# Optimization experiments

Hardware: AMD Instinct MI355X
Metric: run time of the kernel (lower is better)

## Reference

```python
import jax, jax.numpy as jnp
import numpy as np

FP8_MAX = 448.0


def _quantize_fp8(x):
    """Per-tensor symmetric quantization matching the Triton kernel's decode.

    Encode: u = round(clip(x*scale, -448, 448) / 448 * 127)  (stored as u+128 in uint8)
    Decode: x_hat = u / 127 * 448 / scale,  with scale = 448 / amax(|x|).
    We keep u as a float array of integers in [-127, 127] (the +128 uint8 bias
    cancels in the kernel's `u - 128`).
    """
    amax = jnp.max(jnp.abs(x))
    scale = FP8_MAX / jnp.maximum(amax, jnp.asarray(1e-12, x.dtype))
    q = jnp.clip(x * scale, -FP8_MAX, FP8_MAX)
    u = jnp.round(q / FP8_MAX * 127.0)
    return u, scale


def reference(x, weight):
    orig_shape = x.shape
    K = weight.shape[1]
    x2d = x.reshape(-1, K)                      # [M, K]

    ua, a_scale = _quantize_fp8(x2d)            # codes + per-tensor scale
    uw, w_scale = _quantize_fp8(weight)         # weight: [N, K]

    # Kernel dequant: val = u / 127 * FP8_MAX; acc in fp32; rescale by 1/(a_scale*b_scale)
    a_f = ua * (FP8_MAX / 127.0)
    b_f = (uw * (FP8_MAX / 127.0)).T            # [K, N] (weight_fp8.t())
    acc = a_f @ b_f                              # fp32 accumulate, [M, N]
    out = acc * (1.0 / (a_scale * w_scale))
    out = out.astype(x.dtype)
    return out.reshape(*orig_shape[:-1], weight.shape[0])


def setup_inputs() -> dict:
    key = jax.random.key(0)
    k1, k2 = jax.random.split(key)
    x = jax.random.normal(k1, (4, 2048, 4096), dtype=jnp.float32)
    weight = jax.random.normal(k2, (8192, 4096), dtype=jnp.float32) * 0.02
    return {"x": x, "weight": weight}
```

## Files before the change

### kernel.cpp

```cpp
#include <hip/hip_runtime.h>

#define FP8_MAX_F 448.0f

static constexpr int M = 8192;
static constexpr int N = 8192;
static constexpr int K = 4096;

typedef __attribute__((ext_vector_type(4))) int i32x4;

#define AS1 __attribute__((address_space(1)))
#define AS3 __attribute__((address_space(3)))
#define BARRIER() asm volatile("s_barrier" ::: "memory")
#define VMCNT(n)  asm volatile("s_waitcnt vmcnt(" #n ")" ::: "memory")

__global__ void amax_kernel(const float* __restrict__ x, const float* __restrict__ w,
                            unsigned* __restrict__ out) {
    const long n4x = (long)M * K / 4;
    const long n4t = n4x + (long)N * K / 4;
    unsigned lx = 0u, lw = 0u;
    const long stride = (long)gridDim.x * blockDim.x;
    for (long i = (long)blockIdx.x * blockDim.x + threadIdx.x; i < n4t; i += stride) {
        if (i < n4x) {
            float4 v = ((const float4*)x)[i];
            unsigned a0 = __float_as_uint(v.x) & 0x7fffffffu;
            unsigned a1 = __float_as_uint(v.y) & 0x7fffffffu;
            unsigned a2 = __float_as_uint(v.z) & 0x7fffffffu;
            unsigned a3 = __float_as_uint(v.w) & 0x7fffffffu;
            lx = max(lx, max(max(a0, a1), max(a2, a3)));
        } else {
            float4 v = ((const float4*)w)[i - n4x];
            unsigned a0 = __float_as_uint(v.x) & 0x7fffffffu;
            unsigned a1 = __float_as_uint(v.y) & 0x7fffffffu;
            unsigned a2 = __float_as_uint(v.z) & 0x7fffffffu;
            unsigned a3 = __float_as_uint(v.w) & 0x7fffffffu;
            lw = max(lw, max(max(a0, a1), max(a2, a3)));
        }
    }
    #pragma unroll
    for (int off = 32; off > 0; off >>= 1) {
        lx = max(lx, (unsigned)__shfl_down((int)lx, off, 64));
        lw = max(lw, (unsigned)__shfl_down((int)lw, off, 64));
    }
    __shared__ unsigned smx[4], smw[4];
    if ((threadIdx.x & 63) == 0) { smx[threadIdx.x >> 6] = lx; smw[threadIdx.x >> 6] = lw; }
    __syncthreads();
    if (threadIdx.x == 0) {
        atomicMax(&out[0], max(max(smx[0], smx[1]), max(smx[2], smx[3])));
        atomicMax(&out[1], max(max(smw[0], smw[1]), max(smw[2], smw[3])));
    }
}

__device__ __forceinline__ signed char quant1(float v, float s) {
    float f = fminf(fmaxf(v * s, -FP8_MAX_F), FP8_MAX_F);
    return (signed char)(int)rintf(f / FP8_MAX_F * 127.0f);
}

__global__ void quant_kernel(const float* __restrict__ x, const float* __restrict__ w,
                             signed char* __restrict__ qx, signed char* __restrict__ qw,
                             const unsigned* __restrict__ amax_bits) {
    const float ax = fmaxf(__uint_as_float(amax_bits[0]), 1e-12f);
    const float aw = fmaxf(__uint_as_float(amax_bits[1]), 1e-12f);
    const float sxv = FP8_MAX_F / ax;
    const float swv = FP8_MAX_F / aw;
    const long cx = (long)M * K / 16;
    const long ct = cx + (long)N * K / 16;
    const long stride = (long)gridDim.x * blockDim.x;
    for (long ci = (long)blockIdx.x * blockDim.x + threadIdx.x; ci < ct; ci += stride) {
        const float* src; signed char* dst; float s; long c;
        if (ci < cx) { src = x; dst = qx; s = sxv; c = ci; }
        else         { src = w; dst = qw; s = swv; c = ci - cx; }
        const long r = c >> 8;
        const int  cr = (int)(c & 255);
        const float4* in = (const float4*)(src + r * K + cr * 16);
        signed char ob[16];
        #pragma unroll
        for (int j = 0; j < 4; ++j) {
            float4 v = in[j];
            ob[j * 4 + 0] = quant1(v.x, s);
            ob[j * 4 + 1] = quant1(v.y, s);
            ob[j * 4 + 2] = quant1(v.z, s);
            ob[j * 4 + 3] = quant1(v.w, s);
        }
        const int osub = (cr & 3) ^ ((int)(r >> 1) & 3);
        *(int4*)(dst + r * K + ((long)((cr & ~3) + osub)) * 16) = *(const int4*)ob;
    }
}

__global__ __launch_bounds__(512, 2) void gemm_i8_kernel(
    const signed char* __restrict__ Aq, const signed char* __restrict__ Bq,
    float* __restrict__ C, const unsigned* __restrict__ amax_bits)
{
    __shared__ signed char lds[4][2][256 * 64];

    const int tid  = threadIdx.x;
    const int wid  = tid >> 6;
    const int lane = tid & 63;
    const int wm = wid >> 2;
    const int wn = wid & 3;
    const int fr = lane & 15;
    const int fq = lane >> 4;

    const long row0 = (long)blockIdx.x * 256;
    const long col0 = (long)blockIdx.y * 256;

    const signed char* Ablk = Aq + row0 * K;
    const signed char* Bblk = Bq + col0 * K;

    const long stag_off = (long)(tid >> 2) * K + (long)(tid & 3) * 16;

    const int arow = wm * 128 + fr;
    const int aoff = arow * 64 + ((fq ^ ((arow >> 1) & 3)) * 16);
    const int brow = wn * 64 + fr;
    const int boff = brow * 64 + ((fq ^ ((brow >> 1) & 3)) * 16);

    i32x4 acc[8][4] = {};
    i32x4 afR[2][8];
    i32x4 bR[2][4];

#define STAGE_AB(st) do { \
        const signed char* ga = Ablk + (long)(st) * 64 + stag_off; \
        const signed char* gb = Bblk + (long)(st) * 64 + stag_off; \
        signed char* lA = &lds[(st) & 3][0][0]; \
        signed char* lB = &lds[(st) & 3][1][0]; \
        __builtin_amdgcn_global_load_lds((const AS1 void*)ga, \
            (AS3 void*)(lA + wid * 1024), 16, 0, 0); \
        __builtin_amdgcn_global_load_lds((const AS1 void*)(ga + 128L * K), \
            (AS3 void*)(lA + 8192 + wid * 1024), 16, 0, 0); \
        __builtin_amdgcn_global_load_lds((const AS1 void*)gb, \
            (AS3 void*)(lB + wid * 1024), 16, 0, 0); \
        __builtin_amdgcn_global_load_lds((const AS1 void*)(gb + 128L * K), \
            (AS3 void*)(lB + 8192 + wid * 1024), 16, 0, 0); \
    } while (0)

#define READS(t1, NXT) do { \
        const signed char* la = &lds[(t1) & 3][0][0]; \
        const signed char* lb = &lds[(t1) & 3][1][0]; \
        _Pragma("unroll") \
        for (int mi = 0; mi < 8; ++mi) \
            afR[NXT][mi] = *(const i32x4*)(la + aoff + mi * 1024); \
        _Pragma("unroll") \
        for (int ni = 0; ni < 4; ++ni) \
            bR[NXT][ni] = *(const i32x4*)(lb + boff + ni * 1024); \
    } while (0)

#define MFMA32(CUR) do { \
        BARRIER(); \
        __builtin_amdgcn_s_setprio(1); \
        _Pragma("unroll") \
        for (int mi = 0; mi < 8; ++mi) { \
            _Pragma("unroll") \
            for (int ni = 0; ni < 4; ++ni) \
                acc[mi][ni] = __builtin_amdgcn_mfma_i32_16x16x64_i8( \
                    afR[CUR][mi], bR[CUR][ni], acc[mi][ni], 0, 0, 0); \
        } \
        __builtin_amdgcn_s_setprio(0); \
        BARRIER(); \
    } while (0)

    STAGE_AB(0); STAGE_AB(1); STAGE_AB(2);
    VMCNT(4);
    BARRIER();
    READS(0, 0);

    #pragma unroll 1
    for (int t = 0; t < 60; t += 2) {
        READS(t + 1, 1);
        STAGE_AB(t + 3);
        VMCNT(4);
        MFMA32(0);

        READS(t + 2, 0);
        STAGE_AB(t + 4);
        VMCNT(4);
        MFMA32(1);
    }
    READS(61, 1); STAGE_AB(63); VMCNT(4); MFMA32(0);
    READS(62, 0);               VMCNT(0); MFMA32(1);
    READS(63, 1);                         MFMA32(0);
    MFMA32(1);

#undef MFMA32
#undef READS
#undef STAGE_AB

    const float ax = fmaxf(__uint_as_float(amax_bits[0]), 1e-12f);
    const float aw = fmaxf(__uint_as_float(amax_bits[1]), 1e-12f);
    const float factor = ax * aw * (1.0f / (127.0f * 127.0f));

    #pragma unroll
    for (int mi = 0; mi < 8; ++mi) {
        #pragma unroll
        for (int ni = 0; ni < 4; ++ni) {
            const long col = col0 + wn * 64 + ni * 16 + fr;
            #pragma unroll
            for (int j = 0; j < 4; ++j) {
                const long row = row0 + wm * 128 + mi * 16 + fq * 4 + j;
                C[row * N + col] = (float)acc[mi][ni][j] * factor;
            }
        }
    }
}

extern "C" void kernel_launch(void* const* d_in, const int* in_sizes, int n_in,
                              void* d_out, int out_size, void* d_ws, size_t ws_size,
                              hipStream_t stream) {
    const float* x = (const float*)d_in[0];
    const float* w = (const float*)d_in[1];
    float* out = (float*)d_out;

    unsigned char* ws = (unsigned char*)d_ws;
    unsigned* amax = (unsigned*)ws;
    signed char* aq = (signed char*)(ws + 256);
    signed char* wq = aq + (long)M * K;

    hipMemsetAsync(amax, 0, 2 * sizeof(unsigned), stream);
    amax_kernel<<<2048, 256, 0, stream>>>(x, w, amax);
    quant_kernel<<<4096, 256, 0, stream>>>(x, w, aq, wq, amax);

    dim3 grid(M / 256, N / 256);
    gemm_i8_kernel<<<grid, 512, 0, stream>>>(aq, wq, out, amax);
}
```

Baseline: 442.5 us.

## Interleave LDS reads and global stages across four MFMA clusters per tile

Splits each 32-MFMA tile into four 8-MFMA clusters, each with its own barriers. The LDS fragment reads for the next tile and the A/B global-to-LDS stage issues are spread between these clusters instead of being issued in one burst before the MFMA block. Barriers are wrapped in sched_barrier so the compiler cannot move instructions across them. The aim is finer overlap of LDS and global traffic with MFMA work, at the cost of four times as many workgroup barriers per tile.

```diff
diff --git a/kernel.cpp b/kernel.cpp
--- a/kernel.cpp
+++ b/kernel.cpp
@@ -10,7 +10,11 @@
 
 #define AS1 __attribute__((address_space(1)))
 #define AS3 __attribute__((address_space(3)))
-#define BARRIER() asm volatile("s_barrier" ::: "memory")
+#define BARRIER() do { \
+        __builtin_amdgcn_sched_barrier(0); \
+        asm volatile("s_barrier" ::: "memory"); \
+        __builtin_amdgcn_sched_barrier(0); \
+    } while (0)
 #define VMCNT(n)  asm volatile("s_waitcnt vmcnt(" #n ")" ::: "memory")
 
 __global__ void amax_kernel(const float* __restrict__ x, const float* __restrict__ w,
@@ -117,71 +121,96 @@
     i32x4 afR[2][8];
     i32x4 bR[2][4];
 
-#define STAGE_AB(st) do { \
+#define STAGE_A(st) do { \
         const signed char* ga = Ablk + (long)(st) * 64 + stag_off; \
-        const signed char* gb = Bblk + (long)(st) * 64 + stag_off; \
         signed char* lA = &lds[(st) & 3][0][0]; \
-        signed char* lB = &lds[(st) & 3][1][0]; \
         __builtin_amdgcn_global_load_lds((const AS1 void*)ga, \
             (AS3 void*)(lA + wid * 1024), 16, 0, 0); \
         __builtin_amdgcn_global_load_lds((const AS1 void*)(ga + 128L * K), \
             (AS3 void*)(lA + 8192 + wid * 1024), 16, 0, 0); \
+    } while (0)
+
+#define STAGE_B(st) do { \
+        const signed char* gb = Bblk + (long)(st) * 64 + stag_off; \
+        signed char* lB = &lds[(st) & 3][1][0]; \
         __builtin_amdgcn_global_load_lds((const AS1 void*)gb, \
             (AS3 void*)(lB + wid * 1024), 16, 0, 0); \
         __builtin_amdgcn_global_load_lds((const AS1 void*)(gb + 128L * K), \
             (AS3 void*)(lB + 8192 + wid * 1024), 16, 0, 0); \
     } while (0)
 
-#define READS(t1, NXT) do { \
-        const signed char* la = &lds[(t1) & 3][0][0]; \
-        const signed char* lb = &lds[(t1) & 3][1][0]; \
-        _Pragma("unroll") \
-        for (int mi = 0; mi < 8; ++mi) \
-            afR[NXT][mi] = *(const i32x4*)(la + aoff + mi * 1024); \
-        _Pragma("unroll") \
-        for (int ni = 0; ni < 4; ++ni) \
-            bR[NXT][ni] = *(const i32x4*)(lb + boff + ni * 1024); \
-    } while (0)
-
-#define MFMA32(CUR) do { \
+#define CLUSTER(CUR, P) do { \
         BARRIER(); \
         __builtin_amdgcn_s_setprio(1); \
         _Pragma("unroll") \
-        for (int mi = 0; mi < 8; ++mi) { \
-            _Pragma("unroll") \
-            for (int ni = 0; ni < 4; ++ni) \
-                acc[mi][ni] = __builtin_amdgcn_mfma_i32_16x16x64_i8( \
-                    afR[CUR][mi], bR[CUR][ni], acc[mi][ni], 0, 0, 0); \
+        for (int ni = 0; ni < 4; ++ni) { \
+            acc[2*(P)][ni]   = __builtin_amdgcn_mfma_i32_16x16x64_i8( \
+                afR[CUR][2*(P)],   bR[CUR][ni], acc[2*(P)][ni],   0, 0, 0); \
+            acc[2*(P)+1][ni] = __builtin_amdgcn_mfma_i32_16x16x64_i8( \
+                afR[CUR][2*(P)+1], bR[CUR][ni], acc[2*(P)+1][ni], 0, 0, 0); \
         } \
         __builtin_amdgcn_s_setprio(0); \
         BARRIER(); \
     } while (0)
 
-    STAGE_AB(0); STAGE_AB(1); STAGE_AB(2);
+#define TILE_P(CUR, NXT, T1, S0_STMT, S1_STMT, VM_STMT, DO_RD) do { \
+        const signed char* la_ = &lds[(T1) & 3][0][0]; \
+        const signed char* lb_ = &lds[(T1) & 3][1][0]; \
+        if (DO_RD) { \
+            afR[NXT][0] = *(const i32x4*)(la_ + aoff + 0 * 1024); \
+            afR[NXT][1] = *(const i32x4*)(la_ + aoff + 1 * 1024); \
+        } \
+        S0_STMT; \
+        CLUSTER(CUR, 0); \
+        if (DO_RD) { \
+            afR[NXT][2] = *(const i32x4*)(la_ + aoff + 2 * 1024); \
+            afR[NXT][3] = *(const i32x4*)(la_ + aoff + 3 * 1024); \
+            bR[NXT][0]  = *(const i32x4*)(lb_ + boff + 0 * 1024); \
+        } \
+        S1_STMT; \
+        CLUSTER(CUR, 1); \
+        if (DO_RD) { \
+            afR[NXT][4] = *(const i32x4*)(la_ + aoff + 4 * 1024); \
+            afR[NXT][5] = *(const i32x4*)(la_ + aoff + 5 * 1024); \
+            bR[NXT][1]  = *(const i32x4*)(lb_ + boff + 1 * 1024); \
+        } \
+        CLUSTER(CUR, 2); \
+        if (DO_RD) { \
+            afR[NXT][6] = *(const i32x4*)(la_ + aoff + 6 * 1024); \
+            afR[NXT][7] = *(const i32x4*)(la_ + aoff + 7 * 1024); \
+            bR[NXT][2]  = *(const i32x4*)(lb_ + boff + 2 * 1024); \
+            bR[NXT][3]  = *(const i32x4*)(lb_ + boff + 3 * 1024); \
+        } \
+        VM_STMT; \
+        CLUSTER(CUR, 3); \
+    } while (0)
+
+    STAGE_A(0); STAGE_B(0);
+    STAGE_A(1); STAGE_B(1);
+    STAGE_A(2); STAGE_B(2);
     VMCNT(4);
     BARRIER();
-    READS(0, 0);
+    #pragma unroll
+    for (int mi = 0; mi < 8; ++mi)
+        afR[0][mi] = *(const i32x4*)(&lds[0][0][0] + aoff + mi * 1024);
+    #pragma unroll
+    for (int ni = 0; ni < 4; ++ni)
+        bR[0][ni] = *(const i32x4*)(&lds[0][1][0] + boff + ni * 1024);
 
     #pragma unroll 1
     for (int t = 0; t < 60; t += 2) {
-        READS(t + 1, 1);
-        STAGE_AB(t + 3);
-        VMCNT(4);
-        MFMA32(0);
-
-        READS(t + 2, 0);
-        STAGE_AB(t + 4);
-        VMCNT(4);
-        MFMA32(1);
-    }
-    READS(61, 1); STAGE_AB(63); VMCNT(4); MFMA32(0);
-    READS(62, 0);               VMCNT(0); MFMA32(1);
-    READS(63, 1);                         MFMA32(0);
-    MFMA32(1);
-
-#undef MFMA32
-#undef READS
-#undef STAGE_AB
+        TILE_P(0, 1, t + 1, STAGE_A(t + 3), STAGE_B(t + 3), VMCNT(4), 1);
+        TILE_P(1, 0, t + 2, STAGE_A(t + 4), STAGE_B(t + 4), VMCNT(4), 1);
+    }
+    TILE_P(0, 1, 61, STAGE_A(63), STAGE_B(63), VMCNT(4), 1);
+    TILE_P(1, 0, 62, (void)0,     (void)0,     VMCNT(0), 1);
+    TILE_P(0, 1, 63, (void)0,     (void)0,     (void)0,  1);
+    TILE_P(1, 0, 63, (void)0,     (void)0,     (void)0,  0);
+
+#undef TILE_P
+#undef CLUSTER
+#undef STAGE_B
+#undef STAGE_A
 
     const float ax = fmaxf(__uint_as_float(amax_bits[0]), 1e-12f);
     const float aw = fmaxf(__uint_as_float(amax_bits[1]), 1e-12f);
```

New measurement: 419.3 us. 1.06x faster.

## Shrink GEMM tile to 128x256 with double-buffered LDS for higher occupancy

Applied to the files above, without the earlier changes.

The int8 GEMM block tile goes from 256x256 to 128x256, and the 4-stage LDS ring becomes a 2-buffer ping-pong with a simpler stage/read/MFMA step per tile. Launch bounds target 4 blocks per CU, cutting per-wave accumulators from 32 to 16 MFMA tiles so more waves can hide latency. Each step now waits for all loads (vmcnt 0), so less prefetch depth and less data reuse per block. The amax reduction grid is also doubled.

```diff
diff --git a/kernel.cpp b/kernel.cpp
--- a/kernel.cpp
+++ b/kernel.cpp
@@ -86,11 +86,11 @@
     }
 }
 
-__global__ __launch_bounds__(512, 2) void gemm_i8_kernel(
+__global__ __launch_bounds__(512, 4) void gemm_i8_kernel(
     const signed char* __restrict__ Aq, const signed char* __restrict__ Bq,
     float* __restrict__ C, const unsigned* __restrict__ amax_bits)
 {
-    __shared__ signed char lds[4][2][256 * 64];
+    __shared__ signed char lds[2][24576];
 
     const int tid  = threadIdx.x;
     const int wid  = tid >> 6;
@@ -100,101 +100,79 @@
     const int fr = lane & 15;
     const int fq = lane >> 4;
 
-    const long row0 = (long)blockIdx.x * 256;
+    const long row0 = (long)blockIdx.x * 128;
     const long col0 = (long)blockIdx.y * 256;
 
-    const signed char* Ablk = Aq + row0 * K;
-    const signed char* Bblk = Bq + col0 * K;
-
-    const long stag_off = (long)(tid >> 2) * K + (long)(tid & 3) * 16;
-
-    const int arow = wm * 128 + fr;
-    const int aoff = arow * 64 + ((fq ^ ((arow >> 1) & 3)) * 16);
-    const int brow = wn * 64 + fr;
-    const int boff = brow * 64 + ((fq ^ ((brow >> 1) & 3)) * 16);
-
-    i32x4 acc[8][4] = {};
-    i32x4 afR[2][8];
-    i32x4 bR[2][4];
-
-#define STAGE_AB(st) do { \
-        const signed char* ga = Ablk + (long)(st) * 64 + stag_off; \
-        const signed char* gb = Bblk + (long)(st) * 64 + stag_off; \
-        signed char* lA = &lds[(st) & 3][0][0]; \
-        signed char* lB = &lds[(st) & 3][1][0]; \
+    const long stag_row = tid >> 2;
+    const long stag_col = (long)(tid & 3) * 16;
+    const signed char* ga  = Aq + (row0 + stag_row) * K + stag_col;
+    const signed char* gb0 = Bq + (col0 + stag_row) * K + stag_col;
+    const signed char* gb1 = gb0 + 128L * K;
+
+    const int sx = (fq ^ ((fr >> 1) & 3)) * 16;
+    const int aoff = (wm * 64 + fr) * 64 + sx;
+    const int boff = 8192 + (wn * 64 + fr) * 64 + sx;
+
+    i32x4 acc[4][4] = {};
+
+#define STAGE(B) do { \
         __builtin_amdgcn_global_load_lds((const AS1 void*)ga, \
-            (AS3 void*)(lA + wid * 1024), 16, 0, 0); \
-        __builtin_amdgcn_global_load_lds((const AS1 void*)(ga + 128L * K), \
-            (AS3 void*)(lA + 8192 + wid * 1024), 16, 0, 0); \
-        __builtin_amdgcn_global_load_lds((const AS1 void*)gb, \
-            (AS3 void*)(lB + wid * 1024), 16, 0, 0); \
-        __builtin_amdgcn_global_load_lds((const AS1 void*)(gb + 128L * K), \
-            (AS3 void*)(lB + 8192 + wid * 1024), 16, 0, 0); \
+            (AS3 void*)&lds[B][wid * 1024], 16, 0, 0); \
+        __builtin_amdgcn_global_load_lds((const AS1 void*)gb0, \
+            (AS3 void*)&lds[B][8192 + wid * 1024], 16, 0, 0); \
+        __builtin_amdgcn_global_load_lds((const AS1 void*)gb1, \
+            (AS3 void*)&lds[B][16384 + wid * 1024], 16, 0, 0); \
+        ga += 64; gb0 += 64; gb1 += 64; \
     } while (0)
 
-#define READS(t1, NXT) do { \
-        const signed char* la = &lds[(t1) & 3][0][0]; \
-        const signed char* lb = &lds[(t1) & 3][1][0]; \
+#define TILE(B, STAGE_STMT, VM_STMT) do { \
+        STAGE_STMT; \
+        i32x4 af[4], bf[4]; \
         _Pragma("unroll") \
-        for (int mi = 0; mi < 8; ++mi) \
-            afR[NXT][mi] = *(const i32x4*)(la + aoff + mi * 1024); \
+        for (int mi = 0; mi < 4; ++mi) \
+            af[mi] = *(const i32x4*)&lds[B][aoff + mi * 1024]; \
         _Pragma("unroll") \
         for (int ni = 0; ni < 4; ++ni) \
-            bR[NXT][ni] = *(const i32x4*)(lb + boff + ni * 1024); \
-    } while (0)
-
-#define MFMA32(CUR) do { \
-        BARRIER(); \
+            bf[ni] = *(const i32x4*)&lds[B][boff + ni * 1024]; \
         __builtin_amdgcn_s_setprio(1); \
         _Pragma("unroll") \
-        for (int mi = 0; mi < 8; ++mi) { \
+        for (int mi = 0; mi < 4; ++mi) \
             _Pragma("unroll") \
             for (int ni = 0; ni < 4; ++ni) \
                 acc[mi][ni] = __builtin_amdgcn_mfma_i32_16x16x64_i8( \
-                    afR[CUR][mi], bR[CUR][ni], acc[mi][ni], 0, 0, 0); \
-        } \
+                    af[mi], bf[ni], acc[mi][ni], 0, 0, 0); \
         __builtin_amdgcn_s_setprio(0); \
+        VM_STMT; \
         BARRIER(); \
     } while (0)
 
-    STAGE_AB(0); STAGE_AB(1); STAGE_AB(2);
-    VMCNT(4);
+    STAGE(0);
+    VMCNT(0);
     BARRIER();
-    READS(0, 0);
 
     #pragma unroll 1
-    for (int t = 0; t < 60; t += 2) {
-        READS(t + 1, 1);
-        STAGE_AB(t + 3);
-        VMCNT(4);
-        MFMA32(0);
-
-        READS(t + 2, 0);
-        STAGE_AB(t + 4);
-        VMCNT(4);
-        MFMA32(1);
-    }
-    READS(61, 1); STAGE_AB(63); VMCNT(4); MFMA32(0);
-    READS(62, 0);               VMCNT(0); MFMA32(1);
-    READS(63, 1);                         MFMA32(0);
-    MFMA32(1);
-
-#undef MFMA32
-#undef READS
-#undef STAGE_AB
+    for (int t = 0; t < 62; t += 2) {
+        TILE(0, STAGE(1), VMCNT(0));
+        TILE(1, STAGE(0), VMCNT(0));
+    }
+    TILE(0, STAGE(1), VMCNT(0));
+    TILE(1, (void)0,  (void)0);
+
+#undef TILE
+#undef STAGE
 
     const float ax = fmaxf(__uint_as_float(amax_bits[0]), 1e-12f);
     const float aw = fmaxf(__uint_as_float(amax_bits[1]), 1e-12f);
     const float factor = ax * aw * (1.0f / (127.0f * 127.0f));
 
     #pragma unroll
-    for (int mi = 0; mi < 8; ++mi) {
+    for (int mi = 0; mi < 4; ++mi) {
         #pragma unroll
         for (int ni = 0; ni < 4; ++ni) {
             const long col = col0 + wn * 64 + ni * 16 + fr;
             #pragma unroll
             for (int j = 0; j < 4; ++j) {
-                const long row = row0 + wm * 128 + mi * 16 + fq * 4 + j;
+                const long row = row0 + wm * 64 + mi * 16 + fq * 4 + j;
                 C[row * N + col] = (float)acc[mi][ni][j] * factor;
             }
         }
@@ -214,9 +192,9 @@
     signed char* wq = aq + (long)M * K;
 
     hipMemsetAsync(amax, 0, 2 * sizeof(unsigned), stream);
-    amax_kernel<<<2048, 256, 0, stream>>>(x, w, amax);
+    amax_kernel<<<4096, 256, 0, stream>>>(x, w, amax);
     quant_kernel<<<4096, 256, 0, stream>>>(x, w, aq, wq, amax);
 
-    dim3 grid(M / 256, N / 256);
+    dim3 grid(M / 128, N / 256);
     gemm_i8_kernel<<<grid, 512, 0, stream>>>(aq, wq, out, amax);
 }
```

New measurement: 465.9 us. +5.3%, slower.
